# Optimization experiments

Measured on AMD Instinct MI355X. Metric: run time of the kernel, lower is better.

The kernel has to match this reference:

```python
import jax, jax.numpy as jnp
import numpy as np

B, IN, H, K = 4096, 1024, 1024, 32  # batch, input_size, hidden_size, inner_hidden


def setup_inputs() -> dict:
    key = jax.random.key(0)
    ks = jax.random.split(key, 11)
    stdv = 1.0 / np.sqrt(H)
    u = lambda k, shp: jax.random.uniform(k, shp, jnp.float32, -stdv, stdv)
    return {
        "x": jax.random.normal(ks[0], (B, IN), jnp.float32),
        "h_prev": jax.random.normal(ks[1], (B, H), jnp.float32),
        "c_prev": jax.random.normal(ks[2], (B, H), jnp.float32),
        "Wg": u(ks[3], (3 * H, IN + H)),
        "bg": u(ks[4], (3 * H,)),
        "Wc": u(ks[5], (2 * H, IN + H)),
        "bc": u(ks[6], (2 * H,)),
        "W1": u(ks[7], (K, 2)),
        "b1": u(ks[8], (K,)),
        "W2": u(ks[9], (1, K)),
        "b2": u(ks[10], (1,)),
    }


def reference(x, h_prev, c_prev, Wg, bg, Wc, bc, W1, b1, W2, b2):
    combined = jnp.concatenate([x, h_prev], axis=1)          # [B, IN+H]
    gates = combined @ Wg.T + bg                              # [B, 3H]
    i, f, o = jnp.split(jax.nn.sigmoid(gates), 3, axis=1)     # each [B, H]
    cell_raw = combined @ Wc.T + bc                           # [B, 2H]
    pairs = cell_raw.reshape(B, H, 2)                         # [B, H, 2]
    hid = jax.nn.relu(jnp.einsum('bhp,kp->bhk', pairs, W1) + b1)  # [B, H, K]
    g = jnp.einsum('bhk,ok->bho', hid, W2)[..., 0] + b2[0]    # [B, H]
    c_next = f * c_prev + i * g
    h_next = o * jnp.tanh(c_next)
    return (h_next, c_next)
```

## Files before the change

### kernel.cpp

```cpp
#include <hip/hip_runtime.h>
#include <hip/hip_bf16.h>

#define BB   4096
#define INW  1024
#define HH   1024
#define KIN  2048
#define NG   5120
#define KH   32

typedef __bf16 bf16;
typedef __bf16 bf16x4 __attribute__((ext_vector_type(4)));
typedef __bf16 bf16x8 __attribute__((ext_vector_type(8)));
typedef float  floatx4 __attribute__((ext_vector_type(4)));

#define GLD16(gp, lp)                                                          \
  __builtin_amdgcn_global_load_lds(                                            \
      (__attribute__((address_space(1))) const void*)(gp),                     \
      (__attribute__((address_space(3))) void*)(lp), 16, 0, 0)

#define NC4  (BB * KIN / 4)
#define NW8  (NG * KIN / 8)

__global__ __launch_bounds__(256) void prep(
    const float* __restrict__ x, const float* __restrict__ h,
    const float* __restrict__ Wg, const float* __restrict__ Wc,
    bf16* __restrict__ comb, bf16* __restrict__ Wb) {
  int i = blockIdx.x * 256 + threadIdx.x;
  if (i < NC4) {
    int e = i * 4;
    int b = e >> 11;
    int c = e & (KIN - 1);
    const float* src = (c < INW) ? (x + (size_t)b * INW + c)
                                 : (h + (size_t)b * HH + (c - INW));
    float4 v = *(const float4*)src;
    bf16x4 o4;
    o4[0] = (bf16)v.x; o4[1] = (bf16)v.y; o4[2] = (bf16)v.z; o4[3] = (bf16)v.w;
    *(bf16x4*)(comb + e) = o4;
  } else {
    int o = i - NC4;
    if (o < NW8) {
      int lane = o & 63;
      int f    = (o >> 6) & 7;
      int kk   = (o >> 9) & 63;
      int nt   = o >> 15;
      int n = nt * 128 + f * 16 + (lane & 15);
      int k = kk * 32 + (lane >> 4) * 8;
      const float* src = (n < 3 * HH) ? (Wg + (size_t)n * KIN + k)
                                      : (Wc + (size_t)(n - 3 * HH) * KIN + k);
      float4 v0 = *(const float4*)src;
      float4 v1 = *(const float4*)(src + 4);
      bf16x8 ov;
      ov[0] = (bf16)v0.x; ov[1] = (bf16)v0.y; ov[2] = (bf16)v0.z; ov[3] = (bf16)v0.w;
      ov[4] = (bf16)v1.x; ov[5] = (bf16)v1.y; ov[6] = (bf16)v1.z; ov[7] = (bf16)v1.w;
      *(bf16x8*)(Wb + (size_t)o * 8) = ov;
    }
  }
}

__global__ __launch_bounds__(256, 3) void gemm_bt(
    const bf16* __restrict__ A, const bf16* __restrict__ Bm,
    bf16* __restrict__ C) {
  __shared__ bf16 As[128 * 128];

  const int tid  = threadIdx.x;
  const int wave = tid >> 6;
  const int lane = tid & 63;
  const int m0 = blockIdx.x * 128;
  const int nt = blockIdx.y;

  const int wm = (wave >> 1) * 64;
  const int wn = (wave & 1) * 64;
  const int lr = lane & 15;
  const int qd = lane >> 4;

  const bf16* Bq = Bm + (size_t)nt * 262144
                      + (size_t)((wave & 1) * 4) * 512 + (size_t)lane * 8;

  floatx4 acc[4][4] = {};

  for (int kt = 0; kt < KIN / 128; ++kt) {
    bf16x8 bfr[4][4];
#pragma unroll
    for (int ks = 0; ks < 4; ++ks)
#pragma unroll
      for (int ni = 0; ni < 4; ++ni)
        bfr[ks][ni] = *(const bf16x8*)(Bq + (size_t)(((kt * 4 + ks) * 8 + ni) << 9));

    __syncthreads();
#pragma unroll
    for (int j = 0; j < 8; ++j) {
      int q   = j * 256 + tid;
      int row = q >> 4;
      int c   = (q & 15) ^ (row & 15);
      GLD16(A + (size_t)(m0 + row) * KIN + kt * 128 + c * 8,
            As + (size_t)(j * 256 + wave * 64) * 8);
    }
    __syncthreads();

#pragma unroll
    for (int ks = 0; ks < 4; ++ks) {
      bf16x8 af[4];
#pragma unroll
      for (int mi = 0; mi < 4; ++mi) {
        int row  = wm + mi * 16 + lr;
        int slot = (ks * 4 + qd) ^ lr;
        af[mi] = *(const bf16x8*)&As[(row << 7) + (slot << 3)];
      }
#pragma unroll
      for (int mi = 0; mi < 4; ++mi)
#pragma unroll
        for (int ni = 0; ni < 4; ++ni)
          acc[mi][ni] = __builtin_amdgcn_mfma_f32_16x16x32_bf16(
              af[mi], bfr[ks][ni], acc[mi][ni], 0, 0, 0);
    }
  }

#pragma unroll
  for (int mi = 0; mi < 4; ++mi)
#pragma unroll
    for (int ni = 0; ni < 4; ++ni) {
      size_t base = (size_t)(m0 + wm + mi * 16 + qd * 4) * NG
                    + ((size_t)nt * 128 + wn + ni * 16 + lr);
#pragma unroll
      for (int r = 0; r < 4; ++r)
        C[base + (size_t)r * NG] = (bf16)acc[mi][ni][r];
    }
}

__global__ __launch_bounds__(256) void epilogue(
    const bf16* __restrict__ G, const float* __restrict__ c_prev,
    const float* __restrict__ bg, const float* __restrict__ bc,
    const float* __restrict__ W1, const float* __restrict__ b1,
    const float* __restrict__ W2, const float* __restrict__ b2,
    float* __restrict__ h_next, float* __restrict__ c_next) {
  int idx = blockIdx.x * 256 + threadIdx.x;
  int b = idx >> 10;
  int h = idx & (HH - 1);
  const bf16* Gr = G + (size_t)b * NG;

  float gi = (float)Gr[h]          + bg[h];
  float gf = (float)Gr[HH + h]     + bg[HH + h];
  float go = (float)Gr[2 * HH + h] + bg[2 * HH + h];
  float p0 = (float)Gr[3 * HH + 2 * h]     + bc[2 * h];
  float p1 = (float)Gr[3 * HH + 2 * h + 1] + bc[2 * h + 1];

  float g = b2[0];
#pragma unroll
  for (int k = 0; k < KH; ++k) {
    float hv = fmaf(p0, W1[2 * k], fmaf(p1, W1[2 * k + 1], b1[k]));
    hv = fmaxf(hv, 0.0f);
    g = fmaf(hv, W2[k], g);
  }

  float si = 1.0f / (1.0f + __expf(-gi));
  float sf = 1.0f / (1.0f + __expf(-gf));
  float so = 1.0f / (1.0f + __expf(-go));

  float cn = sf * c_prev[idx] + si * g;
  float hn = so * tanhf(cn);
  h_next[idx] = hn;
  c_next[idx] = cn;
}

extern "C" void kernel_launch(void* const* d_in, const int* in_sizes, int n_in,
                              void* d_out, int out_size, void* d_ws, size_t ws_size,
                              hipStream_t stream) {
  const float* x      = (const float*)d_in[0];
  const float* h_prev = (const float*)d_in[1];
  const float* c_prev = (const float*)d_in[2];
  const float* Wg     = (const float*)d_in[3];
  const float* bg     = (const float*)d_in[4];
  const float* Wc     = (const float*)d_in[5];
  const float* bc     = (const float*)d_in[6];
  const float* W1     = (const float*)d_in[7];
  const float* b1     = (const float*)d_in[8];
  const float* W2     = (const float*)d_in[9];
  const float* b2     = (const float*)d_in[10];
  float* out = (float*)d_out;

  char* ws = (char*)d_ws;
  bf16* comb = (bf16*)ws;
  bf16* Wb   = (bf16*)(ws + (size_t)BB * KIN * 2);
  bf16* G    = (bf16*)(ws + (size_t)BB * KIN * 2
                          + (size_t)NG * KIN * 2);

  prep<<<(NC4 + NW8 + 255) / 256, 256, 0, stream>>>(x, h_prev, Wg, Wc, comb, Wb);

  dim3 grid(BB / 128, NG / 128);
  gemm_bt<<<grid, 256, 0, stream>>>(comb, Wb, G);

  epilogue<<<(BB * HH) / 256, 256, 0, stream>>>(
      G, c_prev, bg, bc, W1, b1, W2, b2, out, out + (size_t)BB * HH);
}
```

Before: 255.8 us.

## Fuse LSTM gate epilogue into GEMM via interleaved weight column layout

Reorders the packed bf16 weight matrix so each 128-wide-by-160-column tile holds the i/f/o gate columns and the paired cell columns for the same 32 hidden units. The GEMM can then apply bias, the MLP cell nonlinearity, sigmoids and tanh directly from accumulators and write h_next/c_next. This removes the bf16 intermediate G write/read and the separate epilogue launch, and adds a grouped block swizzle for L2 reuse. In exchange the accumulator tile grows to 4x5 per wave, so register pressure rises, occupancy drops from 3 to 2 blocks, and the MLP loop now runs inside the GEMM kernel.

```diff
diff --git a/kernel.cpp b/kernel.cpp
--- a/kernel.cpp
+++ b/kernel.cpp
@@ -7,6 +7,8 @@
 #define KIN  2048
 #define NG   5120
 #define KH   32
+#define FPG  10
+#define NTG  32
 
 typedef __bf16 bf16;
 typedef __bf16 bf16x4 __attribute__((ext_vector_type(4)));
@@ -40,13 +42,18 @@
     int o = i - NC4;
     if (o < NW8) {
       int lane = o & 63;
-      int f    = (o >> 6) & 7;
-      int kk   = (o >> 9) & 63;
-      int nt   = o >> 15;
-      int n = nt * 128 + f * 16 + (lane & 15);
-      int k = kk * 32 + (lane >> 4) * 8;
-      const float* src = (n < 3 * HH) ? (Wg + (size_t)n * KIN + k)
-                                      : (Wc + (size_t)(n - 3 * HH) * KIN + k);
+      int t    = o >> 6;
+      int f    = t % FPG;
+      t        = t / FPG;
+      int kk   = t & 63;
+      int nt   = t >> 6;
+      int q    = f / 5;
+      int g    = f - q * 5;
+      int hcol = nt * 32 + q * 16 + (lane & 15);
+      int k    = kk * 32 + (lane >> 4) * 8;
+      const float* src = (g < 3)
+          ? (Wg + (size_t)(g * HH + hcol) * KIN + k)
+          : (Wc + (size_t)(2 * hcol + (g - 3)) * KIN + k);
       float4 v0 = *(const float4*)src;
       float4 v1 = *(const float4*)(src + 4);
       bf16x8 ov;
@@ -57,41 +64,48 @@
   }
 }
 
-__global__ __launch_bounds__(256, 3) void gemm_bt(
+__global__ __launch_bounds__(256, 2) void gemm_fused(
     const bf16* __restrict__ A, const bf16* __restrict__ Bm,
-    bf16* __restrict__ C) {
+    const float* __restrict__ c_prev, const float* __restrict__ bg,
+    const float* __restrict__ bc, const float* __restrict__ W1,
+    const float* __restrict__ b1, const float* __restrict__ W2,
+    const float* __restrict__ b2, float* __restrict__ h_next,
+    float* __restrict__ c_next) {
   __shared__ bf16 As[128 * 128];
 
   const int tid  = threadIdx.x;
   const int wave = tid >> 6;
   const int lane = tid & 63;
-  const int m0 = blockIdx.x * 128;
-  const int nt = blockIdx.y;
+
+  const int bid = blockIdx.y * gridDim.x + blockIdx.x;
+  const int swz = (bid & 7) * 128 + (bid >> 3);
+  const int m0  = (swz & 31) * 128;
+  const int nt  = swz >> 5;
 
   const int wm = (wave >> 1) * 64;
-  const int wn = (wave & 1) * 64;
+  const int q  = wave & 1;
   const int lr = lane & 15;
   const int qd = lane >> 4;
 
-  const bf16* Bq = Bm + (size_t)nt * 262144
-                      + (size_t)((wave & 1) * 4) * 512 + (size_t)lane * 8;
-
-  floatx4 acc[4][4] = {};
+  const bf16* Bq = Bm + ((size_t)(nt * 640 + q * 5) * 64 + lane) * 8;
+
+  floatx4 acc[4][5] = {};
 
   for (int kt = 0; kt < KIN / 128; ++kt) {
-    bf16x8 bfr[4][4];
+    bf16x8 bfr[4][5];
 #pragma unroll
     for (int ks = 0; ks < 4; ++ks)
 #pragma unroll
-      for (int ni = 0; ni < 4; ++ni)
-        bfr[ks][ni] = *(const bf16x8*)(Bq + (size_t)(((kt * 4 + ks) * 8 + ni) << 9));
+      for (int ni = 0; ni < 5; ++ni)
+        bfr[ks][ni] =
+            *(const bf16x8*)(Bq + ((size_t)((kt * 4 + ks) * FPG + ni) << 9));
 
     __syncthreads();
 #pragma unroll
     for (int j = 0; j < 8; ++j) {
-      int q   = j * 256 + tid;
-      int row = q >> 4;
-      int c   = (q & 15) ^ (row & 15);
+      int s   = j * 256 + tid;
+      int row = s >> 4;
+      int c   = (s & 15) ^ (row & 15);
       GLD16(A + (size_t)(m0 + row) * KIN + kt * 128 + c * 8,
             As + (size_t)(j * 256 + wave * 64) * 8);
     }
@@ -109,57 +123,55 @@
 #pragma unroll
       for (int mi = 0; mi < 4; ++mi)
 #pragma unroll
-        for (int ni = 0; ni < 4; ++ni)
+        for (int ni = 0; ni < 5; ++ni)
           acc[mi][ni] = __builtin_amdgcn_mfma_f32_16x16x32_bf16(
               af[mi], bfr[ks][ni], acc[mi][ni], 0, 0, 0);
     }
   }
 
+  const int h   = nt * 32 + q * 16 + lr;
+  const float bgi = bg[h];
+  const float bgf = bg[HH + h];
+  const float bgo = bg[2 * HH + h];
+  const float bc0 = bc[2 * h];
+  const float bc1 = bc[2 * h + 1];
+  const float gb  = b2[0];
+
+  float p0[16], p1[16], ga[16];
 #pragma unroll
   for (int mi = 0; mi < 4; ++mi)
 #pragma unroll
-    for (int ni = 0; ni < 4; ++ni) {
-      size_t base = (size_t)(m0 + wm + mi * 16 + qd * 4) * NG
-                    + ((size_t)nt * 128 + wn + ni * 16 + lr);
-#pragma unroll
-      for (int r = 0; r < 4; ++r)
-        C[base + (size_t)r * NG] = (bf16)acc[mi][ni][r];
-    }
-}
-
-__global__ __launch_bounds__(256) void epilogue(
-    const bf16* __restrict__ G, const float* __restrict__ c_prev,
-    const float* __restrict__ bg, const float* __restrict__ bc,
-    const float* __restrict__ W1, const float* __restrict__ b1,
-    const float* __restrict__ W2, const float* __restrict__ b2,
-    float* __restrict__ h_next, float* __restrict__ c_next) {
-  int idx = blockIdx.x * 256 + threadIdx.x;
-  int b = idx >> 10;
-  int h = idx & (HH - 1);
-  const bf16* Gr = G + (size_t)b * NG;
-
-  float gi = (float)Gr[h]          + bg[h];
-  float gf = (float)Gr[HH + h]     + bg[HH + h];
-  float go = (float)Gr[2 * HH + h] + bg[2 * HH + h];
-  float p0 = (float)Gr[3 * HH + 2 * h]     + bc[2 * h];
-  float p1 = (float)Gr[3 * HH + 2 * h + 1] + bc[2 * h + 1];
-
-  float g = b2[0];
+    for (int r = 0; r < 4; ++r) {
+      p0[mi * 4 + r] = acc[mi][3][r] + bc0;
+      p1[mi * 4 + r] = acc[mi][4][r] + bc1;
+      ga[mi * 4 + r] = gb;
+    }
 #pragma unroll
   for (int k = 0; k < KH; ++k) {
-    float hv = fmaf(p0, W1[2 * k], fmaf(p1, W1[2 * k + 1], b1[k]));
-    hv = fmaxf(hv, 0.0f);
-    g = fmaf(hv, W2[k], g);
+    float w0 = W1[2 * k], w1 = W1[2 * k + 1], bk = b1[k], wk = W2[k];
+#pragma unroll
+    for (int e = 0; e < 16; ++e) {
+      float hv = fmaf(p0[e], w0, fmaf(p1[e], w1, bk));
+      hv = fmaxf(hv, 0.0f);
+      ga[e] = fmaf(hv, wk, ga[e]);
+    }
   }
 
-  float si = 1.0f / (1.0f + __expf(-gi));
-  float sf = 1.0f / (1.0f + __expf(-gf));
-  float so = 1.0f / (1.0f + __expf(-go));
-
-  float cn = sf * c_prev[idx] + si * g;
-  float hn = so * tanhf(cn);
-  h_next[idx] = hn;
-  c_next[idx] = cn;
+#pragma unroll
+  for (int mi = 0; mi < 4; ++mi)
+#pragma unroll
+    for (int r = 0; r < 4; ++r) {
+      int b    = m0 + wm + mi * 16 + qd * 4 + r;
+      size_t o = (size_t)b * HH + h;
+      float si = 1.0f / (1.0f + __expf(-(acc[mi][0][r] + bgi)));
+      float sf = 1.0f / (1.0f + __expf(-(acc[mi][1][r] + bgf)));
+      float so = 1.0f / (1.0f + __expf(-(acc[mi][2][r] + bgo)));
+      float cn = fmaf(sf, c_prev[o], si * ga[mi * 4 + r]);
+      float e2 = __expf(2.0f * cn);
+      float th = 1.0f - 2.0f / (e2 + 1.0f);
+      h_next[o] = so * th;
+      c_next[o] = cn;
+    }
 }
 
 extern "C" void kernel_launch(void* const* d_in, const int* in_sizes, int n_in,
@@ -181,14 +193,10 @@
   char* ws = (char*)d_ws;
   bf16* comb = (bf16*)ws;
   bf16* Wb   = (bf16*)(ws + (size_t)BB * KIN * 2);
-  bf16* G    = (bf16*)(ws + (size_t)BB * KIN * 2
-                          + (size_t)NG * KIN * 2);
 
   prep<<<(NC4 + NW8 + 255) / 256, 256, 0, stream>>>(x, h_prev, Wg, Wc, comb, Wb);
 
-  dim3 grid(BB / 128, NG / 128);
-  gemm_bt<<<grid, 256, 0, stream>>>(comb, Wb, G);
-
-  epilogue<<<(BB * HH) / 256, 256, 0, stream>>>(
-      G, c_prev, bg, bc, W1, b1, W2, b2, out, out + (size_t)BB * HH);
+  dim3 grid(BB / 128, NTG);
+  gemm_fused<<<grid, 256, 0, stream>>>(comb, Wb, c_prev, bg, bc, W1, b1, W2,
+                                       b2, out, out + (size_t)BB * HH);
 }
```

After: 236.6 us. -7.5%, faster.
